# Kernel optimization log

Measured on AMD Instinct MI355X. Metric: run time of the kernel, lower is better.

## Reference

```python
import jax, jax.numpy as jnp
import numpy as np
from jax import lax

THRESH = 0.6      # pnet score threshold (threshold[0])
IOU_THR = 0.5     # per-scale nms threshold in detect_face
K_PICKS = 128     # fixed max number of NMS picks (jit-static)
STRIDE = 2.0
CELL = 12.0
NEG = -1e30


def _conv(x, w, b):
    y = lax.conv_general_dilated(x, w, (1, 1), 'VALID',
                                 dimension_numbers=('NCHW', 'OIHW', 'NCHW'))
    return y + b[None, :, None, None]


def _prelu(x, a):
    return jnp.where(x > 0, x, a[None, :, None, None] * x)


def _maxpool2(x):
    return lax.reduce_window(x, -jnp.inf, lax.max, (1, 1, 2, 2), (1, 1, 2, 2), 'VALID')


def _nms(boxes, scores):
    # Greedy union-IoU NMS (nms_numpy math), vectorized with a fixed pick budget.
    # boxes [N,4] (shared grid), scores [N] with invalid entries already = NEG.
    x1, y1, x2, y2 = boxes[:, 0], boxes[:, 1], boxes[:, 2], boxes[:, 3]
    area = (x2 - x1 + 1.0) * (y2 - y1 + 1.0)

    def body(live, _):
        j = jnp.argmax(live)
        s = live[j]
        ok = s > NEG * 0.5
        xx1 = jnp.maximum(x1[j], x1); yy1 = jnp.maximum(y1[j], y1)
        xx2 = jnp.minimum(x2[j], x2); yy2 = jnp.minimum(y2[j], y2)
        inter = jnp.maximum(0.0, xx2 - xx1 + 1.0) * jnp.maximum(0.0, yy2 - yy1 + 1.0)
        iou = inter / (area[j] + area - inter)
        live = jnp.where(iou > IOU_THR, NEG, live).at[j].set(NEG)
        return live, (j, ok)

    _, (idx, ok) = lax.scan(body, scores, None, length=K_PICKS)
    return idx, ok


def setup_inputs():
    key = jax.random.key(0)
    ks = jax.random.split(key, 16)
    B, H, W = 16, 384, 512
    f = lambda k, shp, s=0.1: jax.random.normal(k, shp, jnp.float32) * s
    return {
        'im_data': jax.random.uniform(ks[0], (B, 3, H, W), jnp.float32) * 255.0,
        'c1_w': f(ks[1], (10, 3, 3, 3)), 'c1_b': f(ks[2], (10,)),
        'p1': jnp.full((10,), 0.25, jnp.float32),
        'c2_w': f(ks[3], (16, 10, 3, 3)), 'c2_b': f(ks[4], (16,)),
        'p2': jnp.full((16,), 0.25, jnp.float32),
        'c3_w': f(ks[5], (32, 16, 3, 3)), 'c3_b': f(ks[6], (32,)),
        'p3': jnp.full((32,), 0.25, jnp.float32),
        'c41_w': f(ks[7], (2, 32, 1, 1)), 'c41_b': f(ks[8], (2,)),
        'c42_w': f(ks[9], (4, 32, 1, 1)), 'c42_b': f(ks[10], (4,)),
    }


def reference(im_data, c1_w, c1_b, p1, c2_w, c2_b, p2, c3_w, c3_b, p3,
              c41_w, c41_b, c42_w, c42_b):
    # --- PNet conv trunk (detect_face normalization + MTCNN PNet) ---
    x = (im_data - 127.5) * 0.0078125
    h = _prelu(_conv(x, c1_w, c1_b), p1)
    h = _maxpool2(h)                                   # 2x2 s2 (dims even -> ceil==floor)
    h = _prelu(_conv(h, c2_w, c2_b), p2)
    h = _prelu(_conv(h, c3_w, c3_b), p3)
    probs = jax.nn.softmax(_conv(h, c41_w, c41_b), axis=1)[:, 1]   # [B,Hp,Wp]
    reg = _conv(h, c42_w, c42_b)                                   # [B,4,Hp,Wp]

    # --- generateBoundingBox (dense, masked instead of nonzero; scale=1) ---
    B, Hp, Wp = probs.shape
    yy, xx = jnp.meshgrid(jnp.arange(Hp, dtype=jnp.float32),
                          jnp.arange(Wp, dtype=jnp.float32), indexing='ij')
    boxes4 = jnp.stack([jnp.floor(STRIDE * xx + 1.0).ravel(),
                        jnp.floor(STRIDE * yy + 1.0).ravel(),
                        jnp.floor(STRIDE * xx + CELL).ravel(),
                        jnp.floor(STRIDE * yy + CELL).ravel()], axis=1)  # [N,4]
    scores = probs.reshape(B, -1)                                   # [B,N]
    regf = reg.reshape(B, 4, -1).transpose(0, 2, 1)                 # [B,N,4]
    masked = jnp.where(scores >= THRESH, scores, NEG)

    # --- per-image greedy NMS (batched_nms: images independent) ---
    idx, ok = jax.vmap(_nms, in_axes=(None, 0))(boxes4, masked)     # [B,K]
    pb = boxes4[idx]                                                # [B,K,4]
    ps = jnp.take_along_axis(scores, idx, axis=1)                   # [B,K]
    pr = jnp.take_along_axis(regf, idx[..., None], axis=1)          # [B,K,4]

    w = pb[..., 2] - pb[..., 0]
    hh = pb[..., 3] - pb[..., 1]
    q1 = pb[..., 0] + pr[..., 0] * w
    q2 = pb[..., 1] + pr[..., 1] * hh
    q3 = pb[..., 2] + pr[..., 2] * w
    q4 = pb[..., 3] + pr[..., 3] * hh
    rw = q3 - q1
    rh = q4 - q2
    l = jnp.maximum(rw, rh)
    nx1 = q1 + rw * 0.5 - l * 0.5
    ny1 = q2 + rh * 0.5 - l * 0.5
    out = jnp.stack([nx1, ny1, nx1 + l, ny1 + l, ps], axis=-1)      # [B,K,5]
    return out * ok[..., None].astype(out.dtype)
```

## Files before the change

kernel.cpp:

```cpp
#include <hip/hip_runtime.h>
#include <math.h>

#define BATCH 16
#define IH 384
#define IW 512
#define C1 10
#define P1H 191
#define P1W 255
#define C2 16
#define H2 189
#define W2 253
#define C3 32
#define H3 187
#define W3 251
#define N3 (H3*W3)
#define KP 128
#define CAP 7680
#define NEGV (-1e30f)

typedef _Float16 f16x8 __attribute__((ext_vector_type(8)));
typedef _Float16 f16x4 __attribute__((ext_vector_type(4)));
typedef float    f32x16 __attribute__((ext_vector_type(16)));

#define PXT 66
#define NSUB 2

#define T1R 34
#define T1C 68
__global__ __launch_bounds__(256, 1) void k_conv1pool(
        const float* __restrict__ im, const float* __restrict__ w,
        const float* __restrict__ bia, const float* __restrict__ slope,
        float* __restrict__ outp,
        const float* __restrict__ w3, _Float16* __restrict__ wbuf) {
    __shared__ float T[3 * T1R * T1C];

    int tx = threadIdx.x, ty = threadIdx.y;
    int tid = ty * 16 + tx;
    int bx = blockIdx.x, by = blockIdx.y, bb = blockIdx.z;

    if (bx == 0 && by == 0 && bb == 0) {
        for (int e = tid; e < 4608; e += 256) {
            int oc = e / 144;
            int rem = e - oc * 144;
            int ic = rem / 9;
            int tap = rem - ic * 9;
            float v = w3[e];
            _Float16 h = (_Float16)v;
            _Float16 l = (_Float16)(v - (float)h);
            int d = ((tap * 2 + (ic >> 3)) * 32 + oc) * 8 + (ic & 7);
            wbuf[d] = h;
            wbuf[4608 + d] = l;
        }
    }

    const size_t ibase = (size_t)bb * 3 * IH * IW;
    for (int g = tid; g < 3 * T1R * 33; g += 256) {
        int ch = g / (T1R * 33);
        int rem = g - ch * (T1R * 33);
        int r = rem / 33;
        int c2 = rem - r * 33;
        int yg = 32 * by + r;
        int xg = 64 * bx + 2 * c2;
        float2 v = make_float2(0.f, 0.f);
        if (yg < IH && xg < IW)
            v = *(const float2*)(im + ibase + ((size_t)ch * IH + yg) * IW + xg);
        float2 o;
        o.x = (v.x - 127.5f) * 0.0078125f;
        o.y = (v.y - 127.5f) * 0.0078125f;
        *(float2*)&T[(ch * T1R + r) * T1C + 2 * c2] = o;
    }
    __syncthreads();

    int Y  = by * 16 + ty;
    int X0 = bx * 32 + 2 * tx;
    if (Y >= P1H) return;

    float win[3][4][6];
    #pragma unroll
    for (int ch = 0; ch < 3; ++ch)
        #pragma unroll
        for (int r = 0; r < 4; ++r) {
            const float* p = &T[(ch * T1R + 2 * ty + r) * T1C + 4 * tx];
            float4 a = *(const float4*)p;
            float2 b = *(const float2*)(p + 4);
            win[ch][r][0] = a.x; win[ch][r][1] = a.y;
            win[ch][r][2] = a.z; win[ch][r][3] = a.w;
            win[ch][r][4] = b.x; win[ch][r][5] = b.y;
        }
    #pragma unroll
    for (int ch = 0; ch < 3; ++ch)
        #pragma unroll
        for (int r = 0; r < 4; ++r)
            #pragma unroll
            for (int c = 0; c < 6; ++c)
                asm volatile("" : "+v"(win[ch][r][c]));

    bool px1ok = (X0 + 1 < P1W);
    for (int oc = 0; oc < C1; ++oc) {
        const float* wo = w + oc * 27;
        float bv = bia[oc], sv = slope[oc];
        float c0 = bv, c1 = bv, c2 = bv, c3 = bv;
        float c4 = bv, c5 = bv, c6 = bv, c7 = bv;
        #pragma unroll
        for (int ch = 0; ch < 3; ++ch)
            #pragma unroll
            for (int ky = 0; ky < 3; ++ky)
                #pragma unroll
                for (int kx = 0; kx < 3; ++kx) {
                    float wv = wo[(ch * 3 + ky) * 3 + kx];
                    c0 += win[ch][0 + ky][0 + kx] * wv;
                    c1 += win[ch][0 + ky][1 + kx] * wv;
                    c2 += win[ch][0 + ky][2 + kx] * wv;
                    c3 += win[ch][0 + ky][3 + kx] * wv;
                    c4 += win[ch][1 + ky][0 + kx] * wv;
                    c5 += win[ch][1 + ky][1 + kx] * wv;
                    c6 += win[ch][1 + ky][2 + kx] * wv;
                    c7 += win[ch][1 + ky][3 + kx] * wv;
                }
        float m0 = fmaxf(fmaxf(c0, c1), fmaxf(c4, c5));
        float m1 = fmaxf(fmaxf(c2, c3), fmaxf(c6, c7));
        float p0 = m0 > 0.f ? m0 : sv * m0;
        float p1 = m1 > 0.f ? m1 : sv * m1;
        float* o = outp + (((size_t)bb * C1 + oc) * P1H + Y) * P1W + X0;
        o[0] = p0;
        if (px1ok) o[1] = p1;
    }
}

__global__ __launch_bounds__(256, 1) void k_conv2(
        const float* __restrict__ inp, const float* __restrict__ w,
        const float* __restrict__ bia, const float* __restrict__ slope,
        float* __restrict__ outp) {
    __shared__ __align__(16) float smem[8192];
    float* tile = smem;
    float4* sbuf = (float4*)smem;

    int tx = threadIdx.x, ty = threadIdx.y;
    int tid = ty * 64 + tx;
    int bx = blockIdx.x, byb = blockIdx.y, bb = blockIdx.z;

    const float* pin = inp + (size_t)bb * C1 * P1H * P1W;
    for (int g = tid; g < C1 * 6 * 130; g += 256) {
        int ic = g / 780;
        int rem = g - ic * 780;
        int r = rem / 130;
        int c = rem - r * 130;
        int yg = 4 * byb + r;
        int xg = 128 * bx + c;
        float v = 0.f;
        if (yg < P1H && xg < P1W)
            v = pin[((size_t)ic * P1H + yg) * P1W + xg];
        tile[(ic * 6 + r) * 132 + c] = v;
    }
    __syncthreads();

    int x0 = bx * 128 + tx * 2;
    int y  = byb * 4 + ty;
    bool alive = (x0 < W2) && (y < H2);

    float a0[C2], a1[C2];
    #pragma unroll
    for (int oc = 0; oc < C2; ++oc) { a0[oc] = bia[oc]; a1[oc] = bia[oc]; }

    if (alive) {
        #pragma unroll 1
        for (int ci = 0; ci < C1; ++ci) {
            float v[3][4];
            #pragma unroll
            for (int r = 0; r < 3; ++r) {
                const float* p = &tile[(ci * 6 + ty + r) * 132 + 2 * tx];
                float2 u0 = *(const float2*)p;
                float2 u1 = *(const float2*)(p + 2);
                v[r][0] = u0.x; v[r][1] = u0.y; v[r][2] = u1.x; v[r][3] = u1.y;
            }
            #pragma unroll
            for (int r = 0; r < 3; ++r)
                #pragma unroll
                for (int k = 0; k < 4; ++k)
                    asm volatile("" : "+v"(v[r][k]));
            const float* wc = w + ci * 9;
            #pragma unroll
            for (int oc = 0; oc < C2; ++oc) {
                const float* wo = wc + oc * (C1 * 9);
                float s0 = a0[oc], s1 = a1[oc];
                #pragma unroll
                for (int ky = 0; ky < 3; ++ky)
                    #pragma unroll
                    for (int kx = 0; kx < 3; ++kx) {
                        float wv = wo[ky * 3 + kx];
                        s0 += v[ky][kx]     * wv;
                        s1 += v[ky][kx + 1] * wv;
                    }
                a0[oc] = s0; a1[oc] = s1;
            }
        }
        #pragma unroll
        for (int oc = 0; oc < C2; ++oc) {
            float sl = slope[oc];
            float u0 = a0[oc]; a0[oc] = u0 > 0.f ? u0 : sl * u0;
            float u1 = a1[oc]; a1[oc] = u1 > 0.f ? u1 : sl * u1;
        }
    }
    __syncthreads();

    #pragma unroll
    for (int c4 = 0; c4 < 4; ++c4) {
        int g0 = tid * 8 + c4;
        int p0 = g0 ^ ((g0 >> 3) & 7);
        sbuf[p0] = make_float4(a0[c4 * 4], a0[c4 * 4 + 1], a0[c4 * 4 + 2], a0[c4 * 4 + 3]);
        int g1 = tid * 8 + 4 + c4;
        int p1 = g1 ^ ((g1 >> 3) & 7);
        sbuf[p1] = make_float4(a1[c4 * 4], a1[c4 * 4 + 1], a1[c4 * 4 + 2], a1[c4 * 4 + 3]);
    }
    __syncthreads();

    const size_t obase = (size_t)bb * H2 * W2 * C2;
    #pragma unroll
    for (int it = 0; it < 8; ++it) {
        int g = it * 256 + tid;
        int c4 = g & 3, px = (g >> 2) & 127, ry = g >> 9;
        int xg = bx * 128 + px, yg = byb * 4 + ry;
        if (xg < W2 && yg < H2) {
            int phys = g ^ ((g >> 3) & 7);
            *(float4*)(outp + obase + ((size_t)yg * W2 + xg) * C2 + c4 * 4) = sbuf[phys];
        }
    }
}

__global__ __launch_bounds__(256, 2) void k_conv3mfma(
        const float* __restrict__ act,
        const _Float16* __restrict__ wbuf,
        const float* __restrict__ b3, const float* __restrict__ s3,
        const float* __restrict__ w41, const float* __restrict__ b41,
        const float* __restrict__ w42, const float* __restrict__ b42,
        float* __restrict__ scores, float4* __restrict__ regf) {
    __shared__ __align__(16) _Float16 Ah[6 * 2 * PXT * 8];
    __shared__ __align__(16) _Float16 Al[6 * 2 * PXT * 8];
    __shared__ __align__(16) float    htab[32 * 8];

    int tid = threadIdx.x;
    int bx = blockIdx.x * (NSUB * 32);
    int by = blockIdx.y * 4;
    int bb = blockIdx.z;

    {
        int oc = tid >> 3, f = tid & 7;
        float v;
        if      (f == 0) v = b3[oc];
        else if (f == 1) v = s3[oc];
        else if (f == 2) v = w41[oc];
        else if (f == 3) v = w41[32 + oc];
        else             v = w42[(f - 4) * 32 + oc];
        htab[tid] = v;
    }
    {
        const float* actb = act + (size_t)bb * H2 * W2 * C2;
        for (int e = tid; e < 6 * PXT * 4; e += 256) {
            int ic4 = e & 3;
            int t = e >> 2;
            int px = t % PXT;
            int row = t / PXT;
            int yg = by + row, xg = bx + px;
            float4 v = make_float4(0.f, 0.f, 0.f, 0.f);
            if (yg < H2 && xg < W2)
                v = *(const float4*)(actb + ((size_t)yg * W2 + xg) * C2 + ic4 * 4);
            float xs0 = v.x, xs1 = v.y, xs2 = v.z, xs3 = v.w;
            f16x4 hv, lv;
            _Float16 h;
            h = (_Float16)xs0; hv[0] = h; lv[0] = (_Float16)(xs0 - (float)h);
            h = (_Float16)xs1; hv[1] = h; lv[1] = (_Float16)(xs1 - (float)h);
            h = (_Float16)xs2; hv[2] = h; lv[2] = (_Float16)(xs2 - (float)h);
            h = (_Float16)xs3; hv[3] = h; lv[3] = (_Float16)(xs3 - (float)h);
            int kg = ic4 >> 1, h4 = ic4 & 1;
            int gr = (row * 2 + kg) * PXT + px;
            *(f16x4*)(Ah + gr * 8 + h4 * 4) = hv;
            *(f16x4*)(Al + gr * 8 + h4 * 4) = lv;
        }
    }
    __syncthreads();

    int wv = tid >> 6, lane = tid & 63;
    int col = lane & 31, half = lane >> 5;
    int y = by + wv;
    if (y >= H3) return;

    f32x16 acc[NSUB];
    #pragma unroll
    for (int s = 0; s < NSUB; ++s)
        #pragma unroll
        for (int i = 0; i < 16; ++i) acc[s][i] = 0.f;

    const _Float16* wg = wbuf + (half * 32 + col) * 8;

    #pragma unroll 1
    for (int ky = 0; ky < 3; ++ky) {
        const _Float16* arh = Ah + ((wv + ky) * 2 + half) * (PXT * 8);
        const _Float16* arl = Al + ((wv + ky) * 2 + half) * (PXT * 8);
        #pragma unroll
        for (int kx = 0; kx < 3; ++kx) {
            int tap = ky * 3 + kx;
            f16x8 wh = *(const f16x8*)(wg + tap * 512);
            f16x8 wl = *(const f16x8*)(wg + 4608 + tap * 512);
            #pragma unroll
            for (int s = 0; s < NSUB; ++s) {
                int p = s * 32 + col + kx;
                f16x8 bh = *(const f16x8*)(arh + p * 8);
                f16x8 bl = *(const f16x8*)(arl + p * 8);
                acc[s] = __builtin_amdgcn_mfma_f32_32x32x16_f16(wh, bh, acc[s], 0, 0, 0);
                acc[s] = __builtin_amdgcn_mfma_f32_32x32x16_f16(wl, bh, acc[s], 0, 0, 0);
                acc[s] = __builtin_amdgcn_mfma_f32_32x32x16_f16(wh, bl, acc[s], 0, 0, 0);
            }
        }
    }

    float L0[NSUB], L1[NSUB], R0[NSUB], R1[NSUB], R2[NSUB], R3[NSUB];
    #pragma unroll
    for (int s = 0; s < NSUB; ++s) { L0[s]=0.f; L1[s]=0.f; R0[s]=0.f; R1[s]=0.f; R2[s]=0.f; R3[s]=0.f; }

    #pragma unroll
    for (int r = 0; r < 16; ++r) {
        int oc = (r & 3) + 8 * (r >> 2) + 4 * half;
        float4 t0 = *(const float4*)&htab[oc * 8];
        float4 t1 = *(const float4*)&htab[oc * 8 + 4];
        #pragma unroll
        for (int s = 0; s < NSUB; ++s) {
            float v = acc[s][r] + t0.x;
            v = v > 0.f ? v : v * t0.y;
            L0[s] += v * t0.z; L1[s] += v * t0.w;
            R0[s] += v * t1.x; R1[s] += v * t1.y;
            R2[s] += v * t1.z; R3[s] += v * t1.w;
        }
    }

    float hb0 = b41[0], hb1 = b41[1];
    float rb0 = b42[0], rb1 = b42[1], rb2 = b42[2], rb3 = b42[3];

    #pragma unroll
    for (int s = 0; s < NSUB; ++s) {
        float l0 = L0[s] + __shfl_xor(L0[s], 32) + hb0;
        float l1 = L1[s] + __shfl_xor(L1[s], 32) + hb1;
        float r0 = R0[s] + __shfl_xor(R0[s], 32) + rb0;
        float r1 = R1[s] + __shfl_xor(R1[s], 32) + rb1;
        float r2 = R2[s] + __shfl_xor(R2[s], 32) + rb2;
        float r3 = R3[s] + __shfl_xor(R3[s], 32) + rb3;
        float m = fmaxf(l0, l1);
        float e0 = expf(l0 - m), e1 = expf(l1 - m);
        float p = e1 / (e0 + e1);
        int px = bx + s * 32 + col;
        if (half == 0 && px < W3) {
            size_t n = (size_t)bb * N3 + (size_t)y * W3 + px;
            scores[n] = (p >= 0.6f) ? p : NEGV;
            regf[n] = make_float4(r0, r1, r2, r3);
        }
    }
}

__global__ __launch_bounds__(1024) void k_nms(
        const float* __restrict__ scores, const float4* __restrict__ regf,
        float* __restrict__ outp) {
    __shared__ float s_score[CAP];
    __shared__ int   s_idx[CAP];
    __shared__ float r_s[2][16];
    __shared__ int   r_i[2][16];
    __shared__ float s_picks[KP];
    __shared__ int   s_picki[KP];
    __shared__ int   s_misc[4];

    int tid = threadIdx.x;
    int bb = blockIdx.x;
    const float* sc = scores + (size_t)bb * N3;

    if (tid < 4) s_misc[tid] = 0;
    __syncthreads();

    int cnt = 0;
    for (int i = tid; i < N3; i += 1024) if (sc[i] > 0.f) cnt++;
    atomicAdd(&s_misc[0], cnt);
    __syncthreads();
    int M = s_misc[0];

    int cutbin = 0;
    if (M > CAP) {
        for (int i = tid; i < 2048; i += 1024) s_idx[i] = 0;
        __syncthreads();
        for (int i = tid; i < N3; i += 1024) {
            float s = sc[i];
            if (s > 0.f) {
                int b = (int)((s - 0.6f) * 5120.f);
                b = b < 0 ? 0 : (b > 2047 ? 2047 : b);
                atomicAdd(&s_idx[b], 1);
            }
        }
        __syncthreads();
        if (tid == 0) {
            int accum = 0, b = 2047;
            for (; b >= 0; --b) {
                int c = s_idx[b];
                if (accum + c > CAP) break;
                accum += c;
            }
            s_misc[2] = b + 1;
        }
        __syncthreads();
        cutbin = s_misc[2];
        __syncthreads();
    }

    for (int i = tid; i < N3; i += 1024) {
        float s = sc[i];
        if (s > 0.f) {
            bool keep = true;
            if (M > CAP) {
                int b = (int)((s - 0.6f) * 5120.f);
                b = b < 0 ? 0 : (b > 2047 ? 2047 : b);
                keep = (b >= cutbin);
            }
            if (keep) {
                int pos = atomicAdd(&s_misc[1], 1);
                if (pos < CAP) { s_score[pos] = s; s_idx[pos] = i; }
            }
        }
    }
    __syncthreads();
    int M2 = s_misc[1]; if (M2 > CAP) M2 = CAP;

    int np = 0;
    int   ppi = -1;
    float px1 = 0.f, py1 = 0.f, px2 = 0.f, py2 = 0.f;
    for (int pick = 0; pick < KP; ++pick) {
        float bs = -INFINITY; int bi = 0x7fffffff;
        for (int i = tid; i < M2; i += 1024) {
            float s = s_score[i];
            if (ppi >= 0 && s > NEGV * 0.5f) {
                int id = s_idx[i];
                int cx = id % W3, cy = id / W3;
                float x1 = (float)(2 * cx + 1), y1 = (float)(2 * cy + 1);
                float x2 = (float)(2 * cx + 12), y2 = (float)(2 * cy + 12);
                float xx1 = fmaxf(px1, x1), yy1 = fmaxf(py1, y1);
                float xx2 = fminf(px2, x2), yy2 = fminf(py2, y2);
                float inter = fmaxf(0.f, xx2 - xx1 + 1.f) * fmaxf(0.f, yy2 - yy1 + 1.f);
                float iou = inter / (288.f - inter);
                if (iou > 0.5f) { s = NEGV; s_score[i] = NEGV; }
            }
            int id = s_idx[i];
            if (s > bs || (s == bs && id < bi)) { bs = s; bi = id; }
        }
        #pragma unroll
        for (int off = 32; off; off >>= 1) {
            float os = __shfl_down(bs, off);
            int   oi = __shfl_down(bi, off);
            if (os > bs || (os == bs && oi < bi)) { bs = os; bi = oi; }
        }
        int lane = tid & 63, wv = tid >> 6, buf = pick & 1;
        if (lane == 0) { r_s[buf][wv] = bs; r_i[buf][wv] = bi; }
        __syncthreads();
        if (tid == 0) {
            float ps = r_s[buf][0]; int pi = r_i[buf][0];
            for (int k = 1; k < 16; ++k) {
                float os = r_s[buf][k]; int oi = r_i[buf][k];
                if (os > ps || (os == ps && oi < pi)) { ps = os; pi = oi; }
            }
            s_picks[pick] = ps; s_picki[pick] = pi;
            r_s[buf][0] = ps; r_i[buf][0] = pi;
        }
        __syncthreads();
        float ps = r_s[buf][0]; int pi = r_i[buf][0];
        if (ps < 0.f) break;
        np = pick + 1;

        ppi = pi;
        int pcx = pi % W3, pcy = pi / W3;
        px1 = (float)(2 * pcx + 1);  py1 = (float)(2 * pcy + 1);
        px2 = (float)(2 * pcx + 12); py2 = (float)(2 * pcy + 12);
    }

    if (tid < KP) {
        float* o = outp + ((size_t)bb * KP + tid) * 5;
        if (tid < np) {
            int pi = s_picki[tid]; float ps = s_picks[tid];
            int cx = pi % W3, cy = pi / W3;
            float x1 = (float)(2 * cx + 1), y1 = (float)(2 * cy + 1);
            float x2 = (float)(2 * cx + 12), y2 = (float)(2 * cy + 12);
            float4 r = regf[(size_t)bb * N3 + pi];
            float wd = x2 - x1, hh = y2 - y1;
            float q1 = x1 + r.x * wd, q2 = y1 + r.y * hh;
            float q3 = x2 + r.z * wd, q4 = y2 + r.w * hh;
            float rw = q3 - q1, rh = q4 - q2;
            float L = fmaxf(rw, rh);
            float nx1 = q1 + rw * 0.5f - L * 0.5f;
            float ny1 = q2 + rh * 0.5f - L * 0.5f;
            o[0] = nx1; o[1] = ny1; o[2] = nx1 + L; o[3] = ny1 + L; o[4] = ps;
        } else {
            o[0] = 0.f; o[1] = 0.f; o[2] = 0.f; o[3] = 0.f; o[4] = 0.f;
        }
    }
}

extern "C" void kernel_launch(void* const* d_in, const int* in_sizes, int n_in,
                              void* d_out, int out_size, void* d_ws, size_t ws_size,
                              hipStream_t stream) {
    const float* im   = (const float*)d_in[0];
    const float* c1w  = (const float*)d_in[1];
    const float* c1b  = (const float*)d_in[2];
    const float* p1   = (const float*)d_in[3];
    const float* c2w  = (const float*)d_in[4];
    const float* c2b  = (const float*)d_in[5];
    const float* p2   = (const float*)d_in[6];
    const float* c3w  = (const float*)d_in[7];
    const float* c3b  = (const float*)d_in[8];
    const float* p3   = (const float*)d_in[9];
    const float* c41w = (const float*)d_in[10];
    const float* c41b = (const float*)d_in[11];
    const float* c42w = (const float*)d_in[12];
    const float* c42b = (const float*)d_in[13];

    float* ws = (float*)d_ws;
    const size_t POOL1_FLOATS = (size_t)BATCH * C1 * P1H * P1W;
    float*  pool1  = ws;
    float*  conv2b = ws + POOL1_FLOATS;
    float*  scoresb = ws;
    float4* regfb   = (float4*)(ws + (size_t)BATCH * N3);
    _Float16* wbuf = (_Float16*)d_out;

    k_conv1pool<<<dim3(8, 12, BATCH), dim3(16, 16), 0, stream>>>(im, c1w, c1b, p1, pool1,
                                                                 c3w, wbuf);
    k_conv2   <<<dim3(2, 48, BATCH), dim3(64, 4), 0, stream>>>(pool1, c2w, c2b, p2, conv2b);
    k_conv3mfma<<<dim3(4, 47, BATCH), dim3(256), 0, stream>>>(conv2b, wbuf, c3b, p3,
                                                              c41w, c41b, c42w, c42b,
                                                              scoresb, regfb);
    k_nms<<<dim3(BATCH), dim3(1024), 0, stream>>>(scoresb, regfb, (float*)d_out);
}
```

Baseline: 250.0 us.

## Fuse conv2 into conv3 MFMA kernel, recomputing conv2 halo per tile

Removes the separate conv2 kernel and its global intermediate buffer. The conv3 kernel now loads a pool1 tile into shared memory, computes conv2 plus PReLU for its 6-row by 66-pixel halo, and writes the result straight into the split fp16 hi/lo MFMA operand tiles. The pool1 row stride is padded to 256 so tile loads can use aligned float4 reads. This saves a full round trip of the conv2 activations through global memory and one launch. In exchange, conv2 outputs on tile borders are recomputed, shared memory per block grows, and only 198 of 256 threads do the conv2 work.

```diff
diff --git a/kernel.cpp b/kernel.cpp
--- a/kernel.cpp
+++ b/kernel.cpp
@@ -7,6 +7,7 @@
 #define C1 10
 #define P1H 191
 #define P1W 255
+#define P1S 256
 #define C2 16
 #define H2 189
 #define W2 253
@@ -121,64 +122,89 @@
         float m1 = fmaxf(fmaxf(c2, c3), fmaxf(c6, c7));
         float p0 = m0 > 0.f ? m0 : sv * m0;
         float p1 = m1 > 0.f ? m1 : sv * m1;
-        float* o = outp + (((size_t)bb * C1 + oc) * P1H + Y) * P1W + X0;
+        float* o = outp + (((size_t)bb * C1 + oc) * P1H + Y) * P1S + X0;
         o[0] = p0;
         if (px1ok) o[1] = p1;
     }
 }
 
-__global__ __launch_bounds__(256, 1) void k_conv2(
-        const float* __restrict__ inp, const float* __restrict__ w,
-        const float* __restrict__ bia, const float* __restrict__ slope,
-        float* __restrict__ outp) {
-    __shared__ __align__(16) float smem[8192];
-    float* tile = smem;
-    float4* sbuf = (float4*)smem;
-
-    int tx = threadIdx.x, ty = threadIdx.y;
-    int tid = ty * 64 + tx;
-    int bx = blockIdx.x, byb = blockIdx.y, bb = blockIdx.z;
-
-    const float* pin = inp + (size_t)bb * C1 * P1H * P1W;
-    for (int g = tid; g < C1 * 6 * 130; g += 256) {
-        int ic = g / 780;
-        int rem = g - ic * 780;
-        int r = rem / 130;
-        int c = rem - r * 130;
-        int yg = 4 * byb + r;
-        int xg = 128 * bx + c;
-        float v = 0.f;
-        if (yg < P1H && xg < P1W)
-            v = pin[((size_t)ic * P1H + yg) * P1W + xg];
-        tile[(ic * 6 + r) * 132 + c] = v;
+__global__ __launch_bounds__(256, 2) void k_conv3fused(
+        const float* __restrict__ pool1,
+        const float* __restrict__ w2, const float* __restrict__ b2,
+        const float* __restrict__ s2,
+        const _Float16* __restrict__ wbuf,
+        const float* __restrict__ b3, const float* __restrict__ s3,
+        const float* __restrict__ w41, const float* __restrict__ b41,
+        const float* __restrict__ w42, const float* __restrict__ b42,
+        float* __restrict__ scores, float4* __restrict__ regf) {
+    __shared__ __align__(16) float    Pt[10 * 8 * 68];
+    __shared__ __align__(16) _Float16 Ah[6 * 2 * PXT * 8];
+    __shared__ __align__(16) _Float16 Al[6 * 2 * PXT * 8];
+    __shared__ __align__(16) float    htab[32 * 8];
+
+    int tid = threadIdx.x;
+    int bx = blockIdx.x * (NSUB * 32);
+    int by = blockIdx.y * 4;
+    int bb = blockIdx.z;
+
+    {
+        int oc = tid >> 3, f = tid & 7;
+        float v;
+        if      (f == 0) v = b3[oc];
+        else if (f == 1) v = s3[oc];
+        else if (f == 2) v = w41[oc];
+        else if (f == 3) v = w41[32 + oc];
+        else             v = w42[(f - 4) * 32 + oc];
+        htab[tid] = v;
+    }
+
+    {
+        const float* pin = pool1 + (size_t)bb * C1 * P1H * P1S;
+        for (int g = tid; g < 10 * 8 * 17; g += 256) {
+            int ic = g / 136;
+            int rem = g - ic * 136;
+            int r = rem / 17;
+            int c4 = (rem - r * 17) * 4;
+            int yg = by + r;
+            int xg = bx + c4;
+            float4 v = make_float4(0.f, 0.f, 0.f, 0.f);
+            if (yg < P1H) {
+                const float* src = pin + ((size_t)ic * P1H + yg) * P1S + xg;
+                if (xg + 3 < P1W) v = *(const float4*)src;
+                else {
+                    if (xg     < P1W) v.x = src[0];
+                    if (xg + 1 < P1W) v.y = src[1];
+                    if (xg + 2 < P1W) v.z = src[2];
+                }
+            }
+            *(float4*)&Pt[(ic * 8 + r) * 68 + c4] = v;
+        }
     }
     __syncthreads();
 
-    int x0 = bx * 128 + tx * 2;
-    int y  = byb * 4 + ty;
-    bool alive = (x0 < W2) && (y < H2);
-
-    float a0[C2], a1[C2];
-    #pragma unroll
-    for (int oc = 0; oc < C2; ++oc) { a0[oc] = bia[oc]; a1[oc] = bia[oc]; }
-
-    if (alive) {
+    if (tid < 198) {
+        int r  = tid / 33;
+        int p0 = (tid % 33) * 2;
+        float a0[C2], a1[C2];
+        #pragma unroll
+        for (int oc = 0; oc < C2; ++oc) { a0[oc] = b2[oc]; a1[oc] = b2[oc]; }
+
         #pragma unroll 1
         for (int ci = 0; ci < C1; ++ci) {
             float v[3][4];
             #pragma unroll
-            for (int r = 0; r < 3; ++r) {
-                const float* p = &tile[(ci * 6 + ty + r) * 132 + 2 * tx];
+            for (int rr = 0; rr < 3; ++rr) {
+                const float* p = &Pt[(ci * 8 + r + rr) * 68 + p0];
                 float2 u0 = *(const float2*)p;
                 float2 u1 = *(const float2*)(p + 2);
-                v[r][0] = u0.x; v[r][1] = u0.y; v[r][2] = u1.x; v[r][3] = u1.y;
-            }
-            #pragma unroll
-            for (int r = 0; r < 3; ++r)
+                v[rr][0] = u0.x; v[rr][1] = u0.y; v[rr][2] = u1.x; v[rr][3] = u1.y;
+            }
+            #pragma unroll
+            for (int rr = 0; rr < 3; ++rr)
                 #pragma unroll
                 for (int k = 0; k < 4; ++k)
-                    asm volatile("" : "+v"(v[r][k]));
-            const float* wc = w + ci * 9;
+                    asm volatile("" : "+v"(v[rr][k]));
+            const float* wc = w2 + ci * 9;
             #pragma unroll
             for (int oc = 0; oc < C2; ++oc) {
                 const float* wo = wc + oc * (C1 * 9);
@@ -196,85 +222,30 @@
         }
         #pragma unroll
         for (int oc = 0; oc < C2; ++oc) {
-            float sl = slope[oc];
+            float sl = s2[oc];
             float u0 = a0[oc]; a0[oc] = u0 > 0.f ? u0 : sl * u0;
             float u1 = a1[oc]; a1[oc] = u1 > 0.f ? u1 : sl * u1;
         }
-    }
-    __syncthreads();
-
-    #pragma unroll
-    for (int c4 = 0; c4 < 4; ++c4) {
-        int g0 = tid * 8 + c4;
-        int p0 = g0 ^ ((g0 >> 3) & 7);
-        sbuf[p0] = make_float4(a0[c4 * 4], a0[c4 * 4 + 1], a0[c4 * 4 + 2], a0[c4 * 4 + 3]);
-        int g1 = tid * 8 + 4 + c4;
-        int p1 = g1 ^ ((g1 >> 3) & 7);
-        sbuf[p1] = make_float4(a1[c4 * 4], a1[c4 * 4 + 1], a1[c4 * 4 + 2], a1[c4 * 4 + 3]);
-    }
-    __syncthreads();
-
-    const size_t obase = (size_t)bb * H2 * W2 * C2;
-    #pragma unroll
-    for (int it = 0; it < 8; ++it) {
-        int g = it * 256 + tid;
-        int c4 = g & 3, px = (g >> 2) & 127, ry = g >> 9;
-        int xg = bx * 128 + px, yg = byb * 4 + ry;
-        if (xg < W2 && yg < H2) {
-            int phys = g ^ ((g >> 3) & 7);
-            *(float4*)(outp + obase + ((size_t)yg * W2 + xg) * C2 + c4 * 4) = sbuf[phys];
-        }
-    }
-}
-
-__global__ __launch_bounds__(256, 2) void k_conv3mfma(
-        const float* __restrict__ act,
-        const _Float16* __restrict__ wbuf,
-        const float* __restrict__ b3, const float* __restrict__ s3,
-        const float* __restrict__ w41, const float* __restrict__ b41,
-        const float* __restrict__ w42, const float* __restrict__ b42,
-        float* __restrict__ scores, float4* __restrict__ regf) {
-    __shared__ __align__(16) _Float16 Ah[6 * 2 * PXT * 8];
-    __shared__ __align__(16) _Float16 Al[6 * 2 * PXT * 8];
-    __shared__ __align__(16) float    htab[32 * 8];
-
-    int tid = threadIdx.x;
-    int bx = blockIdx.x * (NSUB * 32);
-    int by = blockIdx.y * 4;
-    int bb = blockIdx.z;
-
-    {
-        int oc = tid >> 3, f = tid & 7;
-        float v;
-        if      (f == 0) v = b3[oc];
-        else if (f == 1) v = s3[oc];
-        else if (f == 2) v = w41[oc];
-        else if (f == 3) v = w41[32 + oc];
-        else             v = w42[(f - 4) * 32 + oc];
-        htab[tid] = v;
-    }
-    {
-        const float* actb = act + (size_t)bb * H2 * W2 * C2;
-        for (int e = tid; e < 6 * PXT * 4; e += 256) {
-            int ic4 = e & 3;
-            int t = e >> 2;
-            int px = t % PXT;
-            int row = t / PXT;
-            int yg = by + row, xg = bx + px;
-            float4 v = make_float4(0.f, 0.f, 0.f, 0.f);
-            if (yg < H2 && xg < W2)
-                v = *(const float4*)(actb + ((size_t)yg * W2 + xg) * C2 + ic4 * 4);
-            float xs0 = v.x, xs1 = v.y, xs2 = v.z, xs3 = v.w;
-            f16x4 hv, lv;
-            _Float16 h;
-            h = (_Float16)xs0; hv[0] = h; lv[0] = (_Float16)(xs0 - (float)h);
-            h = (_Float16)xs1; hv[1] = h; lv[1] = (_Float16)(xs1 - (float)h);
-            h = (_Float16)xs2; hv[2] = h; lv[2] = (_Float16)(xs2 - (float)h);
-            h = (_Float16)xs3; hv[3] = h; lv[3] = (_Float16)(xs3 - (float)h);
-            int kg = ic4 >> 1, h4 = ic4 & 1;
-            int gr = (row * 2 + kg) * PXT + px;
-            *(f16x4*)(Ah + gr * 8 + h4 * 4) = hv;
-            *(f16x4*)(Al + gr * 8 + h4 * 4) = lv;
+        #pragma unroll
+        for (int kg = 0; kg < 2; ++kg) {
+            int gr = (r * 2 + kg) * PXT + p0;
+            #pragma unroll
+            for (int h4 = 0; h4 < 2; ++h4) {
+                f16x4 h0, l0, h1, l1;
+                #pragma unroll
+                for (int j = 0; j < 4; ++j) {
+                    float x0 = a0[kg * 8 + h4 * 4 + j];
+                    _Float16 hh = (_Float16)x0;
+                    h0[j] = hh; l0[j] = (_Float16)(x0 - (float)hh);
+                    float x1 = a1[kg * 8 + h4 * 4 + j];
+                    hh = (_Float16)x1;
+                    h1[j] = hh; l1[j] = (_Float16)(x1 - (float)hh);
+                }
+                *(f16x4*)(Ah + gr * 8 + h4 * 4) = h0;
+                *(f16x4*)(Al + gr * 8 + h4 * 4) = l0;
+                *(f16x4*)(Ah + (gr + 1) * 8 + h4 * 4) = h1;
+                *(f16x4*)(Al + (gr + 1) * 8 + h4 * 4) = l1;
+            }
         }
     }
     __syncthreads();
@@ -515,18 +486,17 @@
     const float* c42b = (const float*)d_in[13];
 
     float* ws = (float*)d_ws;
-    const size_t POOL1_FLOATS = (size_t)BATCH * C1 * P1H * P1W;
-    float*  pool1  = ws;
-    float*  conv2b = ws + POOL1_FLOATS;
-    float*  scoresb = ws;
-    float4* regfb   = (float4*)(ws + (size_t)BATCH * N3);
+    const size_t P1FLOATS = (size_t)BATCH * C1 * P1H * P1S;
+    float*  pool1   = ws;
+    float*  scoresb = ws + P1FLOATS;
+    float4* regfb   = (float4*)(ws + P1FLOATS + (size_t)BATCH * N3);
     _Float16* wbuf = (_Float16*)d_out;
 
     k_conv1pool<<<dim3(8, 12, BATCH), dim3(16, 16), 0, stream>>>(im, c1w, c1b, p1, pool1,
                                                                  c3w, wbuf);
-    k_conv2   <<<dim3(2, 48, BATCH), dim3(64, 4), 0, stream>>>(pool1, c2w, c2b, p2, conv2b);
-    k_conv3mfma<<<dim3(4, 47, BATCH), dim3(256), 0, stream>>>(conv2b, wbuf, c3b, p3,
-                                                              c41w, c41b, c42w, c42b,
-                                                              scoresb, regfb);
+    k_conv3fused<<<dim3(4, 47, BATCH), dim3(256), 0, stream>>>(pool1, c2w, c2b, p2,
+                                                               wbuf, c3b, p3,
+                                                               c41w, c41b, c42w, c42b,
+                                                               scoresb, regfb);
     k_nms<<<dim3(BATCH), dim3(1024), 0, stream>>>(scoresb, regfb, (float*)d_out);
 }
```

Measured after the change: 277.1 us. 10.8% more time.
